# Optimization experiments

Measured on AMD Instinct MI355X. Metric: run time of the kernel, lower is better.

The kernel has to match this reference:

```python
import jax, jax.numpy as jnp
import numpy as np

NUM_USERS = 100000
NUM_ITEMS = 100000
EMB = 64
BATCH = 8192
TEMP = 0.2  # config['temperature']


def _l2norm(x):
    # F.normalize(x, dim=-1): x / max(||x||_2, eps)
    return x / jnp.maximum(jnp.linalg.norm(x, axis=-1, keepdims=True), 1e-12)


def setup_inputs() -> dict:
    key = jax.random.key(0)
    k1, k2, k3, k4, k5 = jax.random.split(key, 5)
    # xavier_uniform bounds for the embedding tables
    bu = float(np.sqrt(6.0 / (NUM_USERS + EMB)))
    bi = float(np.sqrt(6.0 / (NUM_ITEMS + EMB)))
    return {
        "user": jax.random.randint(k1, (BATCH,), 0, NUM_USERS),
        "positive": jax.random.randint(k2, (BATCH,), 0, NUM_ITEMS),
        "negative": jax.random.randint(k3, (BATCH,), 0, NUM_ITEMS),
        "user_emb_weight": jax.random.uniform(k4, (NUM_USERS, EMB), jnp.float32, -bu, bu),
        "item_emb_weight": jax.random.uniform(k5, (NUM_ITEMS, EMB), jnp.float32, -bi, bi),
    }


def reference(user, positive, negative, user_emb_weight, item_emb_weight):
    # encoder == 'MF': raw embedding tables are used directly.
    u = _l2norm(user_emb_weight[user])        # [B, D]
    p = _l2norm(item_emb_weight[positive])    # [B, D]

    # positive ('up') term: per-pair inner products
    ip = jnp.sum(u * p, axis=1)               # [B]
    up = jnp.mean(jnp.log(jnp.exp(ip / TEMP) + jnp.exp(ip * ip / TEMP)))

    # 'down' term. Original computes score over unique(user) x unique(positive)
    # weighted by the outer product of occurrence counts, then takes mean.
    # sum_{unique u,i} c_u*c_i*f(sim(u,i)) == sum over all BxB batch pairs of
    # f(sim(user_b, pos_b')), so we use the full batch cross product (jit-safe)
    # and divide by (#unique users * #unique items) for the mean.
    sim = u @ p.T                              # [B, B]
    score_sum = jnp.sum(jnp.exp(sim / TEMP) + jnp.exp(sim * sim / TEMP))
    nu = jnp.sum(jnp.bincount(user, length=NUM_USERS) > 0).astype(sim.dtype)
    ni = jnp.sum(jnp.bincount(positive, length=NUM_ITEMS) > 0).astype(sim.dtype)
    down = jnp.log(score_sum / (nu * ni))

    # loss_list = [-up, down]
    return jnp.stack([-up, down])
```

## Files before the change

### kernel.cpp

```cpp
#include <hip/hip_runtime.h>
#include <hip/hip_bf16.h>

#define EMB 64

typedef __attribute__((ext_vector_type(8))) short short8;
typedef __attribute__((ext_vector_type(8))) __bf16 bf16x8;
typedef __attribute__((ext_vector_type(4))) float f32x4;

__device__ inline f32x4 mfma16x16x32(short8 a, short8 b, f32x4 c) {
  return __builtin_amdgcn_mfma_f32_16x16x32_bf16(
      __builtin_bit_cast(bf16x8, a), __builtin_bit_cast(bf16x8, b), c, 0, 0, 0);
}

#define EXP2_HW __builtin_amdgcn_exp2f
#define C5LOG2E 7.213475204444817f

__global__ __launch_bounds__(256) void clear_kernel(uint4* __restrict__ p) {
  const int i = blockIdx.x * 256 + threadIdx.x;
  if (i < 12500) p[i] = make_uint4(0u, 0u, 0u, 0u);
}

__global__ __launch_bounds__(256) void prep_kernel(
    const int* __restrict__ user, const int* __restrict__ pos,
    const float* __restrict__ uw, const float* __restrict__ iw,
    __hip_bfloat16* __restrict__ u_bf, __hip_bfloat16* __restrict__ p_bf,
    unsigned char* __restrict__ uflag, unsigned char* __restrict__ iflag,
    float* __restrict__ up_partials)
{
  const int wave = threadIdx.x >> 6;
  const int lane = threadIdx.x & 63;

  float upacc = 0.0f;
  for (int row = blockIdx.x * 4 + wave; row < 8192; row += 2048) {
    const int uidx = user[row];
    const int pidx = pos[row];
    float uv = uw[uidx * EMB + lane];
    float pv = iw[pidx * EMB + lane];

    float us = uv * uv, ps = pv * pv;
    #pragma unroll
    for (int off = 32; off; off >>= 1) {
      us += __shfl_xor(us, off);
      ps += __shfl_xor(ps, off);
    }
    const float un = uv / fmaxf(sqrtf(us), 1e-12f);
    const float pn = pv / fmaxf(sqrtf(ps), 1e-12f);
    u_bf[row * EMB + lane] = __float2bfloat16(un);
    p_bf[row * EMB + lane] = __float2bfloat16(pn);

    float ipv = un * pn;
    #pragma unroll
    for (int off = 32; off; off >>= 1) ipv += __shfl_xor(ipv, off);

    if (lane == 0) {
      uflag[uidx] = 1;
      iflag[pidx] = 1;
      const float t = ipv * C5LOG2E;
      upacc += logf(EXP2_HW(t) + EXP2_HW(ipv * t));
    }
  }

  __shared__ float sred[4];
  if (lane == 0) sred[wave] = upacc;
  __syncthreads();
  if (threadIdx.x == 0)
    up_partials[blockIdx.x] = (sred[0] + sred[1]) + (sred[2] + sred[3]);
}

__global__ __launch_bounds__(256) void gemm_kernel(
    const __hip_bfloat16* __restrict__ U, const __hip_bfloat16* __restrict__ P,
    float* __restrict__ down_partials)
{
  const int by  = blockIdx.x >> 4;
  const int bx0 = (blockIdx.x & 15) << 2;
  const int wave = threadIdx.x >> 6;
  const int lane = threadIdx.x & 63;
  const int r0 = by * 128 + (wave >> 1) * 64;
  const int lrow = lane & 15;
  const int lk   = (lane >> 4) * 8;

  short8 a[4][2];
  #pragma unroll
  for (int i = 0; i < 4; ++i)
    #pragma unroll
    for (int kk = 0; kk < 2; ++kk)
      a[i][kk] = *reinterpret_cast<const short8*>(
          &U[(size_t)(r0 + i * 16 + lrow) * EMB + kk * 32 + lk]);

  float s0 = 0.0f, s1 = 0.0f;

  for (int t = 0; t < 4; ++t) {
    const int c0 = (bx0 + t) * 128 + (wave & 1) * 64;

    short8 b[4][2];
    #pragma unroll
    for (int j = 0; j < 4; ++j)
      #pragma unroll
      for (int kk = 0; kk < 2; ++kk)
        b[j][kk] = *reinterpret_cast<const short8*>(
            &P[(size_t)(c0 + j * 16 + lrow) * EMB + kk * 32 + lk]);

    f32x4 acc[4][4] = {};
    #pragma unroll
    for (int i = 0; i < 4; ++i)
      #pragma unroll
      for (int j = 0; j < 4; ++j) {
        acc[i][j] = mfma16x16x32(a[i][0], b[j][0], acc[i][j]);
        acc[i][j] = mfma16x16x32(a[i][1], b[j][1], acc[i][j]);
      }

    #pragma unroll
    for (int i = 0; i < 4; ++i)
      #pragma unroll
      for (int j = 0; j < 4; ++j)
        #pragma unroll
        for (int r = 0; r < 4; ++r) {
          const float v = acc[i][j][r];
          const float tt = v * C5LOG2E;
          s0 += EXP2_HW(tt);
          s1 += EXP2_HW(v * tt);
        }
  }

  float s = s0 + s1;
  #pragma unroll
  for (int off = 32; off; off >>= 1) s += __shfl_xor(s, off);

  __shared__ float sred[4];
  if (lane == 0) sred[wave] = s;
  __syncthreads();
  if (threadIdx.x == 0)
    down_partials[blockIdx.x] = (sred[0] + sred[1]) + (sred[2] + sred[3]);
}

__global__ __launch_bounds__(1024) void finalize_kernel(
    const float* __restrict__ up_partials, const float* __restrict__ down_partials,
    const uint4* __restrict__ uflag4, const uint4* __restrict__ iflag4,
    float* __restrict__ out)
{
  const int tid  = threadIdx.x;
  const int wave = tid >> 6;
  const int lane = tid & 63;

  float upv = (tid < 512) ? up_partials[tid] : 0.0f;
  float dnv = down_partials[tid];
  int uc = 0, ic = 0;
  for (int i = tid; i < 6250; i += 1024) {
    uint4 v = uflag4[i];
    uc += __popc(v.x) + __popc(v.y) + __popc(v.z) + __popc(v.w);
    uint4 w = iflag4[i];
    ic += __popc(w.x) + __popc(w.y) + __popc(w.z) + __popc(w.w);
  }

  #pragma unroll
  for (int off = 32; off; off >>= 1) {
    upv += __shfl_xor(upv, off);
    dnv += __shfl_xor(dnv, off);
    uc  += __shfl_xor(uc, off);
    ic  += __shfl_xor(ic, off);
  }

  __shared__ float sf[2][16];
  __shared__ int   si[2][16];
  if (lane == 0) { sf[0][wave] = upv; sf[1][wave] = dnv; si[0][wave] = uc; si[1][wave] = ic; }
  __syncthreads();
  if (tid == 0) {
    float usum = 0.0f, dsum = 0.0f; int nu = 0, ni = 0;
    #pragma unroll
    for (int w = 0; w < 16; ++w) {
      usum += sf[0][w]; dsum += sf[1][w]; nu += si[0][w]; ni += si[1][w];
    }
    out[0] = -(usum / 8192.0f);
    out[1] = logf(dsum / ((float)nu * (float)ni));
  }
}

extern "C" void kernel_launch(void* const* d_in, const int* in_sizes, int n_in,
                              void* d_out, int out_size, void* d_ws, size_t ws_size,
                              hipStream_t stream) {
  const int*   user = (const int*)d_in[0];
  const int*   pos  = (const int*)d_in[1];
  const float* uw   = (const float*)d_in[3];
  const float* iw   = (const float*)d_in[4];
  float* out = (float*)d_out;

  char* ws = (char*)d_ws;
  __hip_bfloat16* u_bf = (__hip_bfloat16*)(ws);
  __hip_bfloat16* p_bf = (__hip_bfloat16*)(ws + (1u << 20));
  unsigned char*  uflag = (unsigned char*)(ws + (2u << 20));
  unsigned char*  iflag = uflag + 100000;
  float* up_partials   = (float*)(ws + (2u << 20) + 200000);
  float* down_partials = up_partials + 512;

  clear_kernel<<<49, 256, 0, stream>>>((uint4*)uflag);
  prep_kernel<<<512, 256, 0, stream>>>(user, pos, uw, iw, u_bf, p_bf,
                                       uflag, iflag, up_partials);
  gemm_kernel<<<1024, 256, 0, stream>>>(u_bf, p_bf, down_partials);
  finalize_kernel<<<1, 1024, 0, stream>>>(up_partials, down_partials,
                                          (const uint4*)uflag, (const uint4*)iflag, out);
}
```

Baseline: 45.67 us.

## Count unique ids by first-occurrence scan and shrink GEMM accumulator live range

Unique users and items are now counted by having each row scan all earlier batch indices and count itself only if no earlier duplicate exists. This removes the flag-clearing kernel, the scattered flag writes, and the single-block popcount over 200KB of flags in finalize. The cost is an O(B^2/64) scan of the index arrays inside the prep kernel, whose work grows with row position. The GEMM loop now loads one B fragment at a time with a 4-tile accumulator instead of 16, using four partial sums to cut register pressure and dependency chains.

```diff
diff --git a/kernel.cpp b/kernel.cpp
--- a/kernel.cpp
+++ b/kernel.cpp
@@ -14,24 +14,23 @@
 
 #define EXP2_HW __builtin_amdgcn_exp2f
 #define C5LOG2E 7.213475204444817f
-
-__global__ __launch_bounds__(256) void clear_kernel(uint4* __restrict__ p) {
-  const int i = blockIdx.x * 256 + threadIdx.x;
-  if (i < 12500) p[i] = make_uint4(0u, 0u, 0u, 0u);
-}
 
 __global__ __launch_bounds__(256) void prep_kernel(
     const int* __restrict__ user, const int* __restrict__ pos,
     const float* __restrict__ uw, const float* __restrict__ iw,
     __hip_bfloat16* __restrict__ u_bf, __hip_bfloat16* __restrict__ p_bf,
-    unsigned char* __restrict__ uflag, unsigned char* __restrict__ iflag,
-    float* __restrict__ up_partials)
+    float* __restrict__ up_p, int* __restrict__ uc_p, int* __restrict__ ic_p)
 {
   const int wave = threadIdx.x >> 6;
   const int lane = threadIdx.x & 63;
+  const int blk  = blockIdx.x;
 
   float upacc = 0.0f;
-  for (int row = blockIdx.x * 4 + wave; row < 8192; row += 2048) {
+  int   ucnt = 0, icnt = 0;
+
+  #pragma unroll 1
+  for (int ii = 0; ii < 4; ++ii) {
+    const int row  = blk + (((ii << 2) + wave) << 9);
     const int uidx = user[row];
     const int pidx = pos[row];
     float uv = uw[uidx * EMB + lane];
@@ -53,23 +52,40 @@
     for (int off = 32; off; off >>= 1) ipv += __shfl_xor(ipv, off);
 
     if (lane == 0) {
-      uflag[uidx] = 1;
-      iflag[pidx] = 1;
       const float t = ipv * C5LOG2E;
       upacc += logf(EXP2_HW(t) + EXP2_HW(ipv * t));
     }
-  }
-
-  __shared__ float sred[4];
-  if (lane == 0) sred[wave] = upacc;
+
+    bool udup = false, idup = false;
+    const int nfull = row >> 6;
+    #pragma unroll 4
+    for (int c = 0; c < nfull; ++c) {
+      udup |= (user[(c << 6) + lane] == uidx);
+      idup |= (pos [(c << 6) + lane] == pidx);
+    }
+    const int base = nfull << 6;
+    if (base + lane < row) {
+      udup |= (user[base + lane] == uidx);
+      idup |= (pos [base + lane] == pidx);
+    }
+    ucnt += __any(udup) ? 0 : 1;
+    icnt += __any(idup) ? 0 : 1;
+  }
+
+  __shared__ float sredf[4];
+  __shared__ int   sredu[4], sredi[4];
+  if (lane == 0) { sredf[wave] = upacc; sredu[wave] = ucnt; sredi[wave] = icnt; }
   __syncthreads();
-  if (threadIdx.x == 0)
-    up_partials[blockIdx.x] = (sred[0] + sred[1]) + (sred[2] + sred[3]);
+  if (threadIdx.x == 0) {
+    up_p[blk] = (sredf[0] + sredf[1]) + (sredf[2] + sredf[3]);
+    uc_p[blk] = sredu[0] + sredu[1] + sredu[2] + sredu[3];
+    ic_p[blk] = sredi[0] + sredi[1] + sredi[2] + sredi[3];
+  }
 }
 
 __global__ __launch_bounds__(256) void gemm_kernel(
     const __hip_bfloat16* __restrict__ U, const __hip_bfloat16* __restrict__ P,
-    float* __restrict__ down_partials)
+    float* __restrict__ dn_p)
 {
   const int by  = blockIdx.x >> 4;
   const int bx0 = (blockIdx.x & 15) << 2;
@@ -87,42 +103,39 @@
       a[i][kk] = *reinterpret_cast<const short8*>(
           &U[(size_t)(r0 + i * 16 + lrow) * EMB + kk * 32 + lk]);
 
-  float s0 = 0.0f, s1 = 0.0f;
-
+  float s0 = 0.0f, s1 = 0.0f, s2 = 0.0f, s3 = 0.0f;
+
+  #pragma unroll 2
   for (int t = 0; t < 4; ++t) {
     const int c0 = (bx0 + t) * 128 + (wave & 1) * 64;
-
-    short8 b[4][2];
-    #pragma unroll
-    for (int j = 0; j < 4; ++j)
+    #pragma unroll
+    for (int j = 0; j < 4; ++j) {
+      const short8 b0 = *reinterpret_cast<const short8*>(
+          &P[(size_t)(c0 + j * 16 + lrow) * EMB + lk]);
+      const short8 b1 = *reinterpret_cast<const short8*>(
+          &P[(size_t)(c0 + j * 16 + lrow) * EMB + 32 + lk]);
+
+      f32x4 acc[4] = {};
       #pragma unroll
-      for (int kk = 0; kk < 2; ++kk)
-        b[j][kk] = *reinterpret_cast<const short8*>(
-            &P[(size_t)(c0 + j * 16 + lrow) * EMB + kk * 32 + lk]);
-
-    f32x4 acc[4][4] = {};
-    #pragma unroll
-    for (int i = 0; i < 4; ++i)
+      for (int i = 0; i < 4; ++i) {
+        acc[i] = mfma16x16x32(a[i][0], b0, acc[i]);
+        acc[i] = mfma16x16x32(a[i][1], b1, acc[i]);
+      }
+
       #pragma unroll
-      for (int j = 0; j < 4; ++j) {
-        acc[i][j] = mfma16x16x32(a[i][0], b[j][0], acc[i][j]);
-        acc[i][j] = mfma16x16x32(a[i][1], b[j][1], acc[i][j]);
-      }
-
-    #pragma unroll
-    for (int i = 0; i < 4; ++i)
-      #pragma unroll
-      for (int j = 0; j < 4; ++j)
+      for (int i = 0; i < 4; ++i) {
         #pragma unroll
         for (int r = 0; r < 4; ++r) {
-          const float v = acc[i][j][r];
+          const float v  = acc[i][r];
           const float tt = v * C5LOG2E;
-          s0 += EXP2_HW(tt);
-          s1 += EXP2_HW(v * tt);
+          if (i & 1) { s2 += EXP2_HW(tt); s3 += EXP2_HW(v * tt); }
+          else       { s0 += EXP2_HW(tt); s1 += EXP2_HW(v * tt); }
         }
-  }
-
-  float s = s0 + s1;
+      }
+    }
+  }
+
+  float s = (s0 + s1) + (s2 + s3);
   #pragma unroll
   for (int off = 32; off; off >>= 1) s += __shfl_xor(s, off);
 
@@ -130,27 +143,22 @@
   if (lane == 0) sred[wave] = s;
   __syncthreads();
   if (threadIdx.x == 0)
-    down_partials[blockIdx.x] = (sred[0] + sred[1]) + (sred[2] + sred[3]);
+    dn_p[blockIdx.x] = (sred[0] + sred[1]) + (sred[2] + sred[3]);
 }
 
 __global__ __launch_bounds__(1024) void finalize_kernel(
-    const float* __restrict__ up_partials, const float* __restrict__ down_partials,
-    const uint4* __restrict__ uflag4, const uint4* __restrict__ iflag4,
+    const float* __restrict__ up_p, const float* __restrict__ dn_p,
+    const int* __restrict__ uc_p, const int* __restrict__ ic_p,
     float* __restrict__ out)
 {
   const int tid  = threadIdx.x;
   const int wave = tid >> 6;
   const int lane = tid & 63;
 
-  float upv = (tid < 512) ? up_partials[tid] : 0.0f;
-  float dnv = down_partials[tid];
-  int uc = 0, ic = 0;
-  for (int i = tid; i < 6250; i += 1024) {
-    uint4 v = uflag4[i];
-    uc += __popc(v.x) + __popc(v.y) + __popc(v.z) + __popc(v.w);
-    uint4 w = iflag4[i];
-    ic += __popc(w.x) + __popc(w.y) + __popc(w.z) + __popc(w.w);
-  }
+  float upv = (tid < 512) ? up_p[tid] : 0.0f;
+  float dnv = dn_p[tid];
+  int   uc  = (tid < 512) ? uc_p[tid] : 0;
+  int   ic  = (tid < 512) ? ic_p[tid] : 0;
 
   #pragma unroll
   for (int off = 32; off; off >>= 1) {
@@ -187,15 +195,13 @@
   char* ws = (char*)d_ws;
   __hip_bfloat16* u_bf = (__hip_bfloat16*)(ws);
   __hip_bfloat16* p_bf = (__hip_bfloat16*)(ws + (1u << 20));
-  unsigned char*  uflag = (unsigned char*)(ws + (2u << 20));
-  unsigned char*  iflag = uflag + 100000;
-  float* up_partials   = (float*)(ws + (2u << 20) + 200000);
-  float* down_partials = up_partials + 512;
-
-  clear_kernel<<<49, 256, 0, stream>>>((uint4*)uflag);
+  float* up_p = (float*)(ws + (2u << 20));
+  float* dn_p = up_p + 512;
+  int*   uc_p = (int*)(dn_p + 1024);
+  int*   ic_p = uc_p + 512;
+
   prep_kernel<<<512, 256, 0, stream>>>(user, pos, uw, iw, u_bf, p_bf,
-                                       uflag, iflag, up_partials);
-  gemm_kernel<<<1024, 256, 0, stream>>>(u_bf, p_bf, down_partials);
-  finalize_kernel<<<1, 1024, 0, stream>>>(up_partials, down_partials,
-                                          (const uint4*)uflag, (const uint4*)iflag, out);
-}
+                                       up_p, uc_p, ic_p);
+  gemm_kernel<<<1024, 256, 0, stream>>>(u_bf, p_bf, dn_p);
+  finalize_kernel<<<1, 1024, 0, stream>>>(up_p, dn_p, uc_p, ic_p, out);
+}
```

Result: slower. 54.80 us (+20.0%).

## Vectorize prep rows per quarter-wave and prefetch next B tile in GEMM

Applied to the files above, without the earlier changes.

The prep kernel now handles 16 rows per block, one row per 16-lane group, using float4 loads and 4-wide bf16 stores instead of one scalar element per lane across a loop. The GEMM kernel software-pipelines B loads, issuing the next tile's loads right after the MFMAs so their latency overlaps the exp reduction. It also splits the exp accumulators into four chains to cut the dependency on a single sum. The unroll-1 loop and the redundant wrap-around load on the last iteration add some overhead and register pressure.

```diff
diff --git a/kernel.cpp b/kernel.cpp
--- a/kernel.cpp
+++ b/kernel.cpp
@@ -25,51 +25,67 @@
     const float* __restrict__ uw, const float* __restrict__ iw,
     __hip_bfloat16* __restrict__ u_bf, __hip_bfloat16* __restrict__ p_bf,
     unsigned char* __restrict__ uflag, unsigned char* __restrict__ iflag,
-    float* __restrict__ up_partials)
+    float* __restrict__ up_p)
 {
-  const int wave = threadIdx.x >> 6;
-  const int lane = threadIdx.x & 63;
-
-  float upacc = 0.0f;
-  for (int row = blockIdx.x * 4 + wave; row < 8192; row += 2048) {
-    const int uidx = user[row];
-    const int pidx = pos[row];
-    float uv = uw[uidx * EMB + lane];
-    float pv = iw[pidx * EMB + lane];
-
-    float us = uv * uv, ps = pv * pv;
-    #pragma unroll
-    for (int off = 32; off; off >>= 1) {
-      us += __shfl_xor(us, off);
-      ps += __shfl_xor(ps, off);
-    }
-    const float un = uv / fmaxf(sqrtf(us), 1e-12f);
-    const float pn = pv / fmaxf(sqrtf(ps), 1e-12f);
-    u_bf[row * EMB + lane] = __float2bfloat16(un);
-    p_bf[row * EMB + lane] = __float2bfloat16(pn);
-
-    float ipv = un * pn;
-    #pragma unroll
-    for (int off = 32; off; off >>= 1) ipv += __shfl_xor(ipv, off);
-
-    if (lane == 0) {
-      uflag[uidx] = 1;
-      iflag[pidx] = 1;
-      const float t = ipv * C5LOG2E;
-      upacc += logf(EXP2_HW(t) + EXP2_HW(ipv * t));
-    }
-  }
+  const int tid  = threadIdx.x;
+  const int wave = tid >> 6;
+  const int lane = tid & 63;
+  const int e    = lane & 15;
+  const int row  = blockIdx.x * 16 + wave * 4 + (lane >> 4);
+
+  const int uidx = user[row];
+  const int pidx = pos[row];
+  const float4 uv = *reinterpret_cast<const float4*>(&uw[(size_t)uidx * EMB + e * 4]);
+  const float4 pv = *reinterpret_cast<const float4*>(&iw[(size_t)pidx * EMB + e * 4]);
+
+  float us = uv.x*uv.x + uv.y*uv.y + uv.z*uv.z + uv.w*uv.w;
+  float ps = pv.x*pv.x + pv.y*pv.y + pv.z*pv.z + pv.w*pv.w;
+  #pragma unroll
+  for (int off = 1; off < 16; off <<= 1) {
+    us += __shfl_xor(us, off);
+    ps += __shfl_xor(ps, off);
+  }
+  const float ur = 1.0f / fmaxf(sqrtf(us), 1e-12f);
+  const float pr = 1.0f / fmaxf(sqrtf(ps), 1e-12f);
+  const float4 un = make_float4(uv.x*ur, uv.y*ur, uv.z*ur, uv.w*ur);
+  const float4 pn = make_float4(pv.x*pr, pv.y*pr, pv.z*pr, pv.w*pr);
+
+  ushort4 ub, pb;
+  ub.x = __bfloat16_as_ushort(__float2bfloat16(un.x));
+  ub.y = __bfloat16_as_ushort(__float2bfloat16(un.y));
+  ub.z = __bfloat16_as_ushort(__float2bfloat16(un.z));
+  ub.w = __bfloat16_as_ushort(__float2bfloat16(un.w));
+  pb.x = __bfloat16_as_ushort(__float2bfloat16(pn.x));
+  pb.y = __bfloat16_as_ushort(__float2bfloat16(pn.y));
+  pb.z = __bfloat16_as_ushort(__float2bfloat16(pn.z));
+  pb.w = __bfloat16_as_ushort(__float2bfloat16(pn.w));
+  *reinterpret_cast<ushort4*>(&u_bf[(size_t)row * EMB + e * 4]) = ub;
+  *reinterpret_cast<ushort4*>(&p_bf[(size_t)row * EMB + e * 4]) = pb;
+
+  float ip = un.x*pn.x + un.y*pn.y + un.z*pn.z + un.w*pn.w;
+  #pragma unroll
+  for (int off = 1; off < 16; off <<= 1) ip += __shfl_xor(ip, off);
+
+  float upv = 0.0f;
+  if (e == 0) {
+    uflag[uidx] = 1;
+    iflag[pidx] = 1;
+    const float t = ip * C5LOG2E;
+    upv = logf(EXP2_HW(t) + EXP2_HW(ip * t));
+  }
+  upv += __shfl_xor(upv, 16);
+  upv += __shfl_xor(upv, 32);
 
   __shared__ float sred[4];
-  if (lane == 0) sred[wave] = upacc;
+  if (lane == 0) sred[wave] = upv;
   __syncthreads();
-  if (threadIdx.x == 0)
-    up_partials[blockIdx.x] = (sred[0] + sred[1]) + (sred[2] + sred[3]);
+  if (tid == 0)
+    up_p[blockIdx.x] = (sred[0] + sred[1]) + (sred[2] + sred[3]);
 }
 
 __global__ __launch_bounds__(256) void gemm_kernel(
     const __hip_bfloat16* __restrict__ U, const __hip_bfloat16* __restrict__ P,
-    float* __restrict__ down_partials)
+    float* __restrict__ dn_p)
 {
   const int by  = blockIdx.x >> 4;
   const int bx0 = (blockIdx.x & 15) << 2;
@@ -87,19 +103,22 @@
       a[i][kk] = *reinterpret_cast<const short8*>(
           &U[(size_t)(r0 + i * 16 + lrow) * EMB + kk * 32 + lk]);
 
-  float s0 = 0.0f, s1 = 0.0f;
-
-  for (int t = 0; t < 4; ++t) {
+  short8 b[4][2];
+  auto loadB = [&](int t) {
     const int c0 = (bx0 + t) * 128 + (wave & 1) * 64;
-
-    short8 b[4][2];
     #pragma unroll
     for (int j = 0; j < 4; ++j)
       #pragma unroll
       for (int kk = 0; kk < 2; ++kk)
         b[j][kk] = *reinterpret_cast<const short8*>(
             &P[(size_t)(c0 + j * 16 + lrow) * EMB + kk * 32 + lk]);
-
+  };
+
+  float s0 = 0.0f, s1 = 0.0f, s2 = 0.0f, s3 = 0.0f;
+
+  loadB(0);
+  #pragma unroll 1
+  for (int t = 0; t < 4; ++t) {
     f32x4 acc[4][4] = {};
     #pragma unroll
     for (int i = 0; i < 4; ++i)
@@ -109,20 +128,22 @@
         acc[i][j] = mfma16x16x32(a[i][1], b[j][1], acc[i][j]);
       }
 
+    loadB((t + 1) & 3);
+
     #pragma unroll
     for (int i = 0; i < 4; ++i)
       #pragma unroll
       for (int j = 0; j < 4; ++j)
         #pragma unroll
         for (int r = 0; r < 4; ++r) {
-          const float v = acc[i][j][r];
+          const float v  = acc[i][j][r];
           const float tt = v * C5LOG2E;
-          s0 += EXP2_HW(tt);
-          s1 += EXP2_HW(v * tt);
+          if (j & 1) { s2 += EXP2_HW(tt); s3 += EXP2_HW(v * tt); }
+          else       { s0 += EXP2_HW(tt); s1 += EXP2_HW(v * tt); }
         }
   }
 
-  float s = s0 + s1;
+  float s = (s0 + s1) + (s2 + s3);
   #pragma unroll
   for (int off = 32; off; off >>= 1) s += __shfl_xor(s, off);
 
@@ -130,11 +151,11 @@
   if (lane == 0) sred[wave] = s;
   __syncthreads();
   if (threadIdx.x == 0)
-    down_partials[blockIdx.x] = (sred[0] + sred[1]) + (sred[2] + sred[3]);
+    dn_p[blockIdx.x] = (sred[0] + sred[1]) + (sred[2] + sred[3]);
 }
 
 __global__ __launch_bounds__(1024) void finalize_kernel(
-    const float* __restrict__ up_partials, const float* __restrict__ down_partials,
+    const float* __restrict__ up_p, const float* __restrict__ dn_p,
     const uint4* __restrict__ uflag4, const uint4* __restrict__ iflag4,
     float* __restrict__ out)
 {
@@ -142,8 +163,8 @@
   const int wave = tid >> 6;
   const int lane = tid & 63;
 
-  float upv = (tid < 512) ? up_partials[tid] : 0.0f;
-  float dnv = down_partials[tid];
+  float upv = (tid < 512) ? up_p[tid] : 0.0f;
+  float dnv = dn_p[tid];
   int uc = 0, ic = 0;
   for (int i = tid; i < 6250; i += 1024) {
     uint4 v = uflag4[i];
@@ -187,15 +208,17 @@
   char* ws = (char*)d_ws;
   __hip_bfloat16* u_bf = (__hip_bfloat16*)(ws);
   __hip_bfloat16* p_bf = (__hip_bfloat16*)(ws + (1u << 20));
-  unsigned char*  uflag = (unsigned char*)(ws + (2u << 20));
-  unsigned char*  iflag = uflag + 100000;
-  float* up_partials   = (float*)(ws + (2u << 20) + 200000);
-  float* down_partials = up_partials + 512;
-
-  clear_kernel<<<49, 256, 0, stream>>>((uint4*)uflag);
+  uint4* flag4 = (uint4*)(ws + (2u << 20));
+  unsigned char* uflag = (unsigned char*)flag4;
+  unsigned char* iflag = uflag + 100000;
+  float* up_p = (float*)(ws + (2u << 20) + 200704);
+  float* dn_p = up_p + 512;
+
+  clear_kernel<<<49, 256, 0, stream>>>(flag4);
   prep_kernel<<<512, 256, 0, stream>>>(user, pos, uw, iw, u_bf, p_bf,
-                                       uflag, iflag, up_partials);
-  gemm_kernel<<<1024, 256, 0, stream>>>(u_bf, p_bf, down_partials);
-  finalize_kernel<<<1, 1024, 0, stream>>>(up_partials, down_partials,
-                                          (const uint4*)uflag, (const uint4*)iflag, out);
-}
+                                       uflag, iflag, up_p);
+  gemm_kernel<<<1024, 256, 0, stream>>>(u_bf, p_bf, dn_p);
+  finalize_kernel<<<1, 1024, 0, stream>>>(up_p, dn_p,
+                                          (const uint4*)uflag,
+                                          (const uint4*)iflag, out);
+}
```

After: 45.05 us. Within noise of the previous version (-1.4%).
